# Kernel tuning notes

Hardware: AMD Instinct MI355X
Metric: run time of the kernel (lower is better)

The kernel has to match this reference:

```python
import jax, jax.numpy as jnp
import numpy as np

NUM_HEADS = 4


def setup_inputs() -> dict:
    key = jax.random.key(0)
    ks = jax.random.split(key, 12)
    N, E_edges, ND, ED, D, G = 50000, 800000, 128, 64, 256, 128
    h = jax.random.normal(ks[0], (N, ND), dtype=jnp.float32)
    edge_index = jax.random.randint(ks[1], (2, E_edges), 0, N)
    edge_attr = jax.random.normal(ks[2], (E_edges, ED), dtype=jnp.float32)
    batch = jnp.sort(jax.random.randint(ks[3], (N,), 0, G))
    node_w = jax.random.normal(ks[4], (D, ND), dtype=jnp.float32) / np.sqrt(ND)
    node_b = jnp.zeros((D,), dtype=jnp.float32)
    edge_w = jax.random.normal(ks[5], (D, ED), dtype=jnp.float32) / np.sqrt(ED)
    edge_b = jnp.zeros((D,), dtype=jnp.float32)
    query = jax.random.normal(ks[6], (1, D), dtype=jnp.float32)
    in_w = jax.random.normal(ks[7], (3 * D, D), dtype=jnp.float32) / np.sqrt(D)
    in_b = jnp.zeros((3 * D,), dtype=jnp.float32)
    out_w = jax.random.normal(ks[8], (D, D), dtype=jnp.float32) / np.sqrt(D)
    out_b = jnp.zeros((D,), dtype=jnp.float32)
    return {"h": h, "edge_index": edge_index, "edge_attr": edge_attr, "batch": batch,
            "num_graphs": G, "node_w": node_w, "node_b": node_b,
            "edge_w": edge_w, "edge_b": edge_b, "query": query,
            "in_w": in_w, "in_b": in_b, "out_w": out_w, "out_b": out_b}


def reference(h, edge_index, edge_attr, batch, num_graphs,
              node_w, node_b, edge_w, edge_b, query, in_w, in_b, out_w, out_b):
    N = h.shape[0]
    D = query.shape[-1]
    dh = D // NUM_HEADS
    G = num_graphs
    # node projection
    h_proj = h @ node_w.T + node_b  # [N, D]
    # scatter-mean edge features to source nodes
    row = edge_index[0]
    e_proj = edge_attr @ edge_w.T + edge_b  # [E, D]
    e_sum = jax.ops.segment_sum(e_proj, row, num_segments=N)
    cnt = jax.ops.segment_sum(jnp.ones((row.shape[0],), jnp.float32), row, num_segments=N)
    h_proj = h_proj + e_sum / jnp.maximum(cnt, 1.0)[:, None]
    # per-graph single-query multi-head attention (torch MultiheadAttention math)
    wq, wk, wv = in_w[:D], in_w[D:2 * D], in_w[2 * D:]
    bq, bk, bv = in_b[:D], in_b[D:2 * D], in_b[2 * D:]
    q = (query @ wq.T + bq).reshape(NUM_HEADS, dh)            # [H, dh]
    k = (h_proj @ wk.T + bk).reshape(N, NUM_HEADS, dh)        # [N, H, dh]
    v = (h_proj @ wv.T + bv).reshape(N, NUM_HEADS, dh)        # [N, H, dh]
    scores = jnp.einsum('hd,nhd->nh', q, k) / jnp.sqrt(jnp.float32(dh))  # [N, H]
    smax = jax.ops.segment_max(scores, batch, num_segments=G)  # [G, H]
    w = jnp.exp(scores - smax[batch])                          # [N, H]
    denom = jax.ops.segment_sum(w, batch, num_segments=G)      # [G, H]
    p = w / jnp.maximum(denom[batch], 1e-30)                   # [N, H]
    pooled = jax.ops.segment_sum(p[:, :, None] * v, batch, num_segments=G)  # [G, H, dh]
    out = pooled.reshape(G, 1, D) @ out_w.T + out_b            # [G, 1, D]
    return out
```

## Files before the change

kernel.cpp:

```cpp
#include <hip/hip_runtime.h>
#include <hip/hip_bf16.h>
#include <math.h>

#define NDIM 128
#define EDIM 64
#define DDIM 256
#define BM 32
#define APK_STRIDE 204
#define HPB_STRIDE 264
#define NSPLIT 4
#define CAP 96
#define NSWZ (8 * 12 * 64 * 8)

typedef __attribute__((ext_vector_type(8))) short short8;
typedef __attribute__((ext_vector_type(16))) float floatx16;

__device__ inline ushort f2bf(float x) {
    uint32_t u = __float_as_uint(x);
    uint32_t r = (u + 0x7fff + ((u >> 16) & 1)) >> 16;
    return (ushort)r;
}
__device__ inline float bf2f(ushort h) { return __uint_as_float(((uint32_t)h) << 16); }
__device__ inline uint32_t pack_hilo(float x) {
    ushort hi = f2bf(x);
    ushort lo = f2bf(x - bf2f(hi));
    return (uint32_t)hi | ((uint32_t)lo << 16);
}

__global__ __launch_bounds__(256) void k_setup(
    int* __restrict__ zero_p, int n_zero, int ZBLK,
    const float* __restrict__ node_w, const float* __restrict__ edge_w,
    ushort* __restrict__ whi, ushort* __restrict__ wlo,
    const float* __restrict__ query, const float* __restrict__ in_w,
    const float* __restrict__ in_b, float* __restrict__ qk, float* __restrict__ sb)
{
    const int tid = threadIdx.x;
    int b = blockIdx.x;
    if (b < ZBLK) {
        int i = b * 256 + tid;
        if (i < n_zero) zero_p[i] = 0;
        return;
    }
    b -= ZBLK;
    if (b < 192) {
        int idx = b * 256 + tid;
        int i = idx & 7;
        int l = (idx >> 3) & 63;
        int rest = idx >> 9;
        int s = rest % 12;
        int t2 = rest / 12;
        int k = s * 16 + (l >> 5) * 8 + i;
        int col = t2 * 32 + (l & 31);
        float val = (k < NDIM) ? node_w[(size_t)col * NDIM + k]
                               : edge_w[(size_t)col * EDIM + (k - NDIM)];
        ushort hi = f2bf(val);
        ushort lo = f2bf(val - bf2f(hi));
        whi[idx] = hi;
        wlo[idx] = lo;
        return;
    }
    __shared__ float q_s[DDIM];
    __shared__ float qv[DDIM];
    q_s[tid] = query[tid];
    __syncthreads();
    float acc = in_b[tid];
    const float* wq = in_w + (size_t)tid * DDIM;
    for (int i = 0; i < DDIM; ++i) acc += q_s[i] * wq[i];
    qv[tid] = acc;
    __syncthreads();
    for (int h = 0; h < 4; ++h) {
        float a = 0.f;
        for (int d = 0; d < 64; ++d)
            a += qv[h * 64 + d] * in_w[(size_t)(DDIM + h * 64 + d) * DDIM + tid];
        qk[h * DDIM + tid] = a;
    }
    if (tid < 4) {
        float a = 0.f;
        for (int d = 0; d < 64; ++d) a += qv[tid * 64 + d] * in_b[DDIM + tid * 64 + d];
        sb[tid] = a;
    }
}

__global__ __launch_bounds__(256) void k_scatter(
    const int* __restrict__ erow, int* __restrict__ fill,
    int* __restrict__ perm, int E)
{
    int e = blockIdx.x * 256 + threadIdx.x;
    if (e < E) {
        int r = erow[e];
        int pos = atomicAdd(&fill[r], 1);
        if (pos < CAP) perm[(size_t)r * CAP + pos] = e;
    }
}

__global__ __launch_bounds__(256) void k_agg(
    const float* __restrict__ edge_attr, const int* __restrict__ perm,
    const int* __restrict__ fill, float* __restrict__ agg, int N)
{
    int tid = threadIdx.x;
    int n = blockIdx.x * 4 + (tid >> 6);
    if (n >= N) return;
    int lane = tid & 63, seg = lane & 15, jg = lane >> 4;
    int s = n * CAP;
    int c = min(fill[n], CAP);
    float4 acc = make_float4(0.f, 0.f, 0.f, 0.f);
    int j = jg;
    for (; j + 12 < c; j += 16) {
        int e0 = perm[s + j];
        int e1 = perm[s + j + 4];
        int e2 = perm[s + j + 8];
        int e3 = perm[s + j + 12];
        float4 a0 = *reinterpret_cast<const float4*>(edge_attr + (size_t)e0 * EDIM + seg * 4);
        float4 a1 = *reinterpret_cast<const float4*>(edge_attr + (size_t)e1 * EDIM + seg * 4);
        float4 a2 = *reinterpret_cast<const float4*>(edge_attr + (size_t)e2 * EDIM + seg * 4);
        float4 a3 = *reinterpret_cast<const float4*>(edge_attr + (size_t)e3 * EDIM + seg * 4);
        acc.x += (a0.x + a1.x) + (a2.x + a3.x);
        acc.y += (a0.y + a1.y) + (a2.y + a3.y);
        acc.z += (a0.z + a1.z) + (a2.z + a3.z);
        acc.w += (a0.w + a1.w) + (a2.w + a3.w);
    }
    for (; j < c; j += 4) {
        int e0 = perm[s + j];
        float4 a0 = *reinterpret_cast<const float4*>(edge_attr + (size_t)e0 * EDIM + seg * 4);
        acc.x += a0.x; acc.y += a0.y; acc.z += a0.z; acc.w += a0.w;
    }
#pragma unroll
    for (int off = 16; off < 64; off <<= 1) {
        acc.x += __shfl_xor(acc.x, off);
        acc.y += __shfl_xor(acc.y, off);
        acc.z += __shfl_xor(acc.z, off);
        acc.w += __shfl_xor(acc.w, off);
    }
    if (jg == 0)
        *reinterpret_cast<float4*>(agg + (size_t)n * EDIM + seg * 4) = acc;
}

__global__ __launch_bounds__(256) void k_proj_mfma(
    const float* __restrict__ h, const float* __restrict__ agg, const int* __restrict__ fill,
    const ushort* __restrict__ whi, const ushort* __restrict__ wlo,
    const float* __restrict__ node_b, const float* __restrict__ edge_b,
    const float* __restrict__ qk, const float* __restrict__ sb,
    ushort* __restrict__ h_proj_bf, float* __restrict__ scores, int N)
{
    extern __shared__ char smem[];
    uint32_t* A_pk = (uint32_t*)smem;
    ushort*   hpbuf = (ushort*)smem;
    __shared__ float qk_s[4 * DDIM];
    __shared__ float cnt_s[BM];
    __shared__ float sb_s[4];

    const int tid = threadIdx.x;
    const int n0 = blockIdx.x * BM;

    if (tid < BM) {
        int n = n0 + tid;
        cnt_s[tid] = (n < N) ? (float)fill[n] : 0.f;
    }
    if (tid < 4) sb_s[tid] = sb[tid];
    for (int i = tid; i < 4 * DDIM; i += 256) qk_s[i] = qk[i];
    __syncthreads();

    const float4* h4 = reinterpret_cast<const float4*>(h);
#pragma unroll
    for (int it = 0; it < 4; ++it) {
        int idx4 = tid + 256 * it;
        int node = idx4 >> 5;
        int kq = idx4 & 31;
        float4 v = make_float4(0.f, 0.f, 0.f, 0.f);
        if (n0 + node < N) v = h4[(size_t)(n0 + node) * 32 + kq];
        uint32_t* dst = &A_pk[node * APK_STRIDE + kq * 4];
        dst[0] = pack_hilo(v.x); dst[1] = pack_hilo(v.y);
        dst[2] = pack_hilo(v.z); dst[3] = pack_hilo(v.w);
    }
    const float4* a4 = reinterpret_cast<const float4*>(agg);
#pragma unroll
    for (int it = 0; it < 2; ++it) {
        int idx4 = tid + 256 * it;
        int node = idx4 >> 4;
        int kq = idx4 & 15;
        float4 v = make_float4(0.f, 0.f, 0.f, 0.f);
        if (n0 + node < N) v = a4[(size_t)(n0 + node) * 16 + kq];
        float inv = 1.f / fmaxf(cnt_s[node], 1.f);
        uint32_t* dst = &A_pk[node * APK_STRIDE + NDIM + kq * 4];
        dst[0] = pack_hilo(v.x * inv); dst[1] = pack_hilo(v.y * inv);
        dst[2] = pack_hilo(v.z * inv); dst[3] = pack_hilo(v.w * inv);
    }
    __syncthreads();

    const int lane = tid & 63;
    const int w = tid >> 6;
    const int kg8 = (lane >> 5) * 8;
    const uint32_t* arow_p = &A_pk[(lane & 31) * APK_STRIDE];

    floatx16 acc[2];
#pragma unroll
    for (int t = 0; t < 2; ++t) acc[t] = 0.f;

#pragma unroll 4
    for (int s = 0; s < 12; ++s) {
        uint32_t au[8];
        *reinterpret_cast<uint4*>(&au[0]) = *reinterpret_cast<const uint4*>(&arow_p[s * 16 + kg8]);
        *reinterpret_cast<uint4*>(&au[4]) = *reinterpret_cast<const uint4*>(&arow_p[s * 16 + kg8 + 4]);
        short8 ahi, alo;
#pragma unroll
        for (int j = 0; j < 8; ++j) {
            ahi[j] = (short)(au[j] & 0xffffu);
            alo[j] = (short)(au[j] >> 16);
        }
#pragma unroll
        for (int t = 0; t < 2; ++t) {
            size_t boff = ((size_t)(((w * 2 + t) * 12 + s) * 64) + lane) * 8;
            short8 bhi = *reinterpret_cast<const short8*>(whi + boff);
            short8 blo = *reinterpret_cast<const short8*>(wlo + boff);
            acc[t] = __builtin_amdgcn_mfma_f32_32x32x16_bf16(ahi, bhi, acc[t], 0, 0, 0);
            acc[t] = __builtin_amdgcn_mfma_f32_32x32x16_bf16(ahi, blo, acc[t], 0, 0, 0);
            acc[t] = __builtin_amdgcn_mfma_f32_32x32x16_bf16(alo, bhi, acc[t], 0, 0, 0);
        }
    }
    __syncthreads();

#pragma unroll
    for (int t = 0; t < 2; ++t) {
        int colt = (w * 2 + t) * 32 + (lane & 31);
        float nb = node_b[colt];
        float eb = edge_b[colt];
#pragma unroll
        for (int r = 0; r < 16; ++r) {
            int row = (r & 3) + 8 * (r >> 2) + 4 * (lane >> 5);
            float fl = (cnt_s[row] >= 0.5f) ? 1.f : 0.f;
            float hp = acc[t][r] + nb + fl * eb;
            hpbuf[row * HPB_STRIDE + colt] = f2bf(hp);
        }
    }
    __syncthreads();

    {
        int row = tid >> 3, seg = tid & 7;
        int n = n0 + row;
        float s0 = 0.f, s1 = 0.f, s2 = 0.f, s3 = 0.f;
#pragma unroll
        for (int q = 0; q < 4; ++q) {
            short8 v = *reinterpret_cast<const short8*>(
                &hpbuf[row * HPB_STRIDE + seg * 32 + q * 8]);
#pragma unroll
            for (int jj = 0; jj < 8; ++jj) {
                float hv = bf2f((ushort)v[jj]);
                int dim = seg * 32 + q * 8 + jj;
                s0 += hv * qk_s[0 * DDIM + dim];
                s1 += hv * qk_s[1 * DDIM + dim];
                s2 += hv * qk_s[2 * DDIM + dim];
                s3 += hv * qk_s[3 * DDIM + dim];
            }
            if (n < N)
                *reinterpret_cast<short8*>(
                    &h_proj_bf[(size_t)n * DDIM + seg * 32 + q * 8]) = v;
        }
#pragma unroll
        for (int off = 1; off < 8; off <<= 1) {
            s0 += __shfl_xor(s0, off);
            s1 += __shfl_xor(s1, off);
            s2 += __shfl_xor(s2, off);
            s3 += __shfl_xor(s3, off);
        }
        if (seg == 0 && n < N) {
            scores[(size_t)n * 4 + 0] = (s0 + sb_s[0]) * 0.125f;
            scores[(size_t)n * 4 + 1] = (s1 + sb_s[1]) * 0.125f;
            scores[(size_t)n * 4 + 2] = (s2 + sb_s[2]) * 0.125f;
            scores[(size_t)n * 4 + 3] = (s3 + sb_s[3]) * 0.125f;
        }
    }
}

__global__ __launch_bounds__(256) void k_pool2(
    const ushort* __restrict__ h_proj_bf, const float* __restrict__ scores,
    const int* __restrict__ batch,
    float* __restrict__ pm, float* __restrict__ pd, float* __restrict__ phb, int N)
{
    __shared__ float sc_s[256 * 4];
    __shared__ float red_s[16];
    __shared__ float red[4][4][DDIM];

    const int b = blockIdx.x;
    const int g = b >> 2;
    const int part = b & 3;
    const int tid = threadIdx.x;
    const int lane = tid & 63;
    const int wave = tid >> 6;
    const int ng = tid >> 6;
    const int d0 = (tid & 63) * 4;

    int lo = 0, hi = N;
    while (lo < hi) { int mid = (lo + hi) >> 1; if (batch[mid] < g) lo = mid + 1; else hi = mid; }
    const int s = lo;
    hi = N;
    while (lo < hi) { int mid = (lo + hi) >> 1; if (batch[mid] < g + 1) lo = mid + 1; else hi = mid; }
    const int e = lo;
    const int len = e - s;
    const int cs = s + (len * part) / NSPLIT;
    const int ce = s + (len * (part + 1)) / NSPLIT;

    float m[4], dn[4];
    float hbv[4][4];
#pragma unroll
    for (int hh = 0; hh < 4; ++hh) {
        m[hh] = -INFINITY; dn[hh] = 0.f;
#pragma unroll
        for (int d = 0; d < 4; ++d) hbv[hh][d] = 0.f;
    }

    const int h = tid & 3;

    for (int c = cs; c < ce; c += 256) {
        int cn = min(256, ce - c);
        __syncthreads();
        if (tid < cn)
            *reinterpret_cast<float4*>(&sc_s[tid * 4]) =
                *reinterpret_cast<const float4*>(scores + (size_t)(c + tid) * 4);
        __syncthreads();

        float lm = -INFINITY;
        for (int n = tid >> 2; n < cn; n += 64) lm = fmaxf(lm, sc_s[n * 4 + h]);
#pragma unroll
        for (int off = 4; off < 64; off <<= 1) lm = fmaxf(lm, __shfl_xor(lm, off));
        if (lane < 4) red_s[wave * 4 + lane] = lm;
        __syncthreads();

        float nm[4];
#pragma unroll
        for (int hh = 0; hh < 4; ++hh) {
            float cm = fmaxf(fmaxf(red_s[hh], red_s[4 + hh]),
                             fmaxf(red_s[8 + hh], red_s[12 + hh]));
            nm[hh] = fmaxf(m[hh], cm);
            float sc = expf(m[hh] - nm[hh]);
            dn[hh] *= sc;
#pragma unroll
            for (int d = 0; d < 4; ++d) hbv[hh][d] *= sc;
            m[hh] = nm[hh];
        }
        __syncthreads();

        float mh = (h == 0) ? nm[0] : (h == 1) ? nm[1] : (h == 2) ? nm[2] : nm[3];
        float ld = 0.f;
        for (int idx = tid; idx < cn * 4; idx += 256) {
            float wv = expf(sc_s[idx] - mh);
            sc_s[idx] = wv;
            ld += wv;
        }
#pragma unroll
        for (int off = 4; off < 64; off <<= 1) ld += __shfl_xor(ld, off);
        __syncthreads();
        if (lane < 4) red_s[wave * 4 + lane] = ld;
        __syncthreads();
#pragma unroll
        for (int hh = 0; hh < 4; ++hh)
            dn[hh] += red_s[hh] + red_s[4 + hh] + red_s[8 + hh] + red_s[12 + hh];

#pragma unroll 2
        for (int nb = 0; nb < cn; nb += 4) {
            int ln = nb + ng;
            bool valid = ln < cn;
            float4 w4 = make_float4(0.f, 0.f, 0.f, 0.f);
            ushort4 hv = make_ushort4(0, 0, 0, 0);
            if (valid) {
                w4 = *reinterpret_cast<const float4*>(&sc_s[ln * 4]);
                hv = *reinterpret_cast<const ushort4*>(
                    &h_proj_bf[(size_t)(c + ln) * DDIM + d0]);
            }
            float vx = bf2f(hv.x), vy = bf2f(hv.y), vz = bf2f(hv.z), vw = bf2f(hv.w);
            hbv[0][0] += w4.x * vx; hbv[1][0] += w4.y * vx; hbv[2][0] += w4.z * vx; hbv[3][0] += w4.w * vx;
            hbv[0][1] += w4.x * vy; hbv[1][1] += w4.y * vy; hbv[2][1] += w4.z * vy; hbv[3][1] += w4.w * vy;
            hbv[0][2] += w4.x * vz; hbv[1][2] += w4.y * vz; hbv[2][2] += w4.z * vz; hbv[3][2] += w4.w * vz;
            hbv[0][3] += w4.x * vw; hbv[1][3] += w4.y * vw; hbv[2][3] += w4.z * vw; hbv[3][3] += w4.w * vw;
        }
    }

    __syncthreads();
#pragma unroll
    for (int hh = 0; hh < 4; ++hh)
#pragma unroll
        for (int d = 0; d < 4; ++d)
            red[ng][hh][d0 + d] = hbv[hh][d];
    __syncthreads();

    if (tid < 4) { pm[b * 4 + tid] = m[tid]; pd[b * 4 + tid] = dn[tid]; }
#pragma unroll
    for (int hh = 0; hh < 4; ++hh)
        phb[(size_t)(b * 4 + hh) * DDIM + tid] =
            red[0][hh][tid] + red[1][hh][tid] + red[2][hh][tid] + red[3][hh][tid];
}

__global__ __launch_bounds__(256) void k_out(
    const float* __restrict__ pm, const float* __restrict__ pd, const float* __restrict__ phb,
    const float* __restrict__ in_w, const float* __restrict__ in_b,
    const float* __restrict__ out_w, const float* __restrict__ out_b,
    float* __restrict__ out)
{
    __shared__ float hb_s[4 * DDIM];
    __shared__ float po_s[DDIM];

    const int g = blockIdx.x;
    const int tid = threadIdx.x;
    const int b0 = NSPLIT * g;

    float M[4], dnm[4], sc[NSPLIT][4];
#pragma unroll
    for (int hh = 0; hh < 4; ++hh) {
        float Mh = -INFINITY;
#pragma unroll
        for (int p = 0; p < NSPLIT; ++p) Mh = fmaxf(Mh, pm[(b0 + p) * 4 + hh]);
        M[hh] = Mh;
        float d = 0.f;
#pragma unroll
        for (int p = 0; p < NSPLIT; ++p) {
            float mp = pm[(b0 + p) * 4 + hh];
            float scp = (mp == -INFINITY) ? 0.f : expf(mp - Mh);
            sc[p][hh] = scp;
            d += pd[(b0 + p) * 4 + hh] * scp;
        }
        dnm[hh] = d;
    }
    const float has = (M[0] > -INFINITY) ? 1.f : 0.f;

#pragma unroll
    for (int hh = 0; hh < 4; ++hh) {
        float hb = 0.f;
#pragma unroll
        for (int p = 0; p < NSPLIT; ++p)
            hb += phb[(size_t)((b0 + p) * 4 + hh) * DDIM + tid] * sc[p][hh];
        hb_s[hh * DDIM + tid] = hb / fmaxf(dnm[hh], 1e-30f);
    }
    __syncthreads();

    const int jh = tid >> 6;
    const float* wv_row = in_w + (size_t)(2 * DDIM + tid) * DDIM;
    const float* hbr = &hb_s[jh * DDIM];
    float p = 0.f;
    for (int i = 0; i < DDIM; i += 4) {
        float4 a = *reinterpret_cast<const float4*>(hbr + i);
        float4 bb = *reinterpret_cast<const float4*>(wv_row + i);
        p += a.x * bb.x + a.y * bb.y + a.z * bb.z + a.w * bb.w;
    }
    p = (p + in_b[2 * DDIM + tid]) * has;
    po_s[tid] = p;
    __syncthreads();

    const float* ow_row = out_w + (size_t)tid * DDIM;
    float o = out_b[tid];
    for (int i = 0; i < DDIM; i += 4) {
        float4 a = *reinterpret_cast<const float4*>(&po_s[i]);
        float4 bb = *reinterpret_cast<const float4*>(ow_row + i);
        o += a.x * bb.x + a.y * bb.y + a.z * bb.z + a.w * bb.w;
    }
    out[(size_t)g * DDIM + tid] = o;
}

extern "C" void kernel_launch(void* const* d_in, const int* in_sizes, int n_in,
                              void* d_out, int out_size, void* d_ws, size_t ws_size,
                              hipStream_t stream) {
    const float* h         = (const float*)d_in[0];
    const int*   edge_idx  = (const int*)d_in[1];
    const float* edge_attr = (const float*)d_in[2];
    const int*   batch     = (const int*)d_in[3];
    const float* node_w    = (const float*)d_in[5];
    const float* node_b    = (const float*)d_in[6];
    const float* edge_w    = (const float*)d_in[7];
    const float* edge_b    = (const float*)d_in[8];
    const float* query     = (const float*)d_in[9];
    const float* in_w      = (const float*)d_in[10];
    const float* in_b      = (const float*)d_in[11];
    const float* out_w     = (const float*)d_in[12];
    const float* out_b     = (const float*)d_in[13];
    float* out = (float*)d_out;

    const int N = in_sizes[0] / NDIM;
    const int E = in_sizes[2] / EDIM;
    const int G = out_size / DDIM;

    char* ws = (char*)d_ws;
    size_t off = 0;
    auto alloc = [&](size_t bytes) { void* p = ws + off; off += (bytes + 255) & ~(size_t)255; return p; };

    int*    fill       = (int*)alloc((size_t)N * 4);
    int*    perm       = (int*)alloc((size_t)N * CAP * 4);
    float*  agg        = (float*)alloc((size_t)N * EDIM * 4);
    ushort* h_proj_bf  = (ushort*)alloc((size_t)N * DDIM * 2);
    float*  scores     = (float*)alloc((size_t)N * 4 * 4);
    ushort* whi        = (ushort*)alloc((size_t)NSWZ * 2);
    ushort* wlo        = (ushort*)alloc((size_t)NSWZ * 2);
    float*  qk         = (float*)alloc(4 * DDIM * 4);
    float*  sb         = (float*)alloc(16 * 4);
    float*  pm         = (float*)alloc((size_t)NSPLIT * G * 4 * 4);
    float*  pd         = (float*)alloc((size_t)NSPLIT * G * 4 * 4);
    float*  phb        = (float*)alloc((size_t)NSPLIT * G * 4 * DDIM * 4);

    const int ZBLK = (N + 255) / 256;
    k_setup<<<ZBLK + 192 + 1, 256, 0, stream>>>(
        fill, N, ZBLK, node_w, edge_w, whi, wlo, query, in_w, in_b, qk, sb);

    k_scatter<<<(E + 255) / 256, 256, 0, stream>>>(edge_idx, fill, perm, E);
    k_agg<<<(N + 3) / 4, 256, 0, stream>>>(edge_attr, perm, fill, agg, N);

    const int ldsA = BM * APK_STRIDE * 4;
    k_proj_mfma<<<(N + BM - 1) / BM, 256, ldsA, stream>>>(
        h, agg, fill, whi, wlo, node_b, edge_b, qk, sb, h_proj_bf, scores, N);

    k_pool2<<<NSPLIT * G, 256, 0, stream>>>(h_proj_bf, scores, batch, pm, pd, phb, N);
    k_out<<<G, 256, 0, stream>>>(pm, pd, phb, in_w, in_b, out_w, out_b, out);
}
```

Measured before the change: 206.2 us.

## Fuse edge-feature gather aggregation into the MFMA projection kernel

Removes the separate k_agg kernel and the agg intermediate buffer. The projection kernel now gathers each node's incoming edge rows through perm directly, with 8 threads per node each summing 8 columns, and writes the mean straight into shared memory. This saves one launch plus the write and reread of an N×64 float buffer. In exchange, the gather loses the 4-way edge-parallel split per node, so per-thread loops are longer, latency hiding in a kernel with heavy shared-memory use may be weaker, and load imbalance comes from varying degree.

```diff
diff --git a/kernel.cpp b/kernel.cpp
--- a/kernel.cpp
+++ b/kernel.cpp
@@ -93,50 +93,9 @@
     }
 }
 
-__global__ __launch_bounds__(256) void k_agg(
-    const float* __restrict__ edge_attr, const int* __restrict__ perm,
-    const int* __restrict__ fill, float* __restrict__ agg, int N)
-{
-    int tid = threadIdx.x;
-    int n = blockIdx.x * 4 + (tid >> 6);
-    if (n >= N) return;
-    int lane = tid & 63, seg = lane & 15, jg = lane >> 4;
-    int s = n * CAP;
-    int c = min(fill[n], CAP);
-    float4 acc = make_float4(0.f, 0.f, 0.f, 0.f);
-    int j = jg;
-    for (; j + 12 < c; j += 16) {
-        int e0 = perm[s + j];
-        int e1 = perm[s + j + 4];
-        int e2 = perm[s + j + 8];
-        int e3 = perm[s + j + 12];
-        float4 a0 = *reinterpret_cast<const float4*>(edge_attr + (size_t)e0 * EDIM + seg * 4);
-        float4 a1 = *reinterpret_cast<const float4*>(edge_attr + (size_t)e1 * EDIM + seg * 4);
-        float4 a2 = *reinterpret_cast<const float4*>(edge_attr + (size_t)e2 * EDIM + seg * 4);
-        float4 a3 = *reinterpret_cast<const float4*>(edge_attr + (size_t)e3 * EDIM + seg * 4);
-        acc.x += (a0.x + a1.x) + (a2.x + a3.x);
-        acc.y += (a0.y + a1.y) + (a2.y + a3.y);
-        acc.z += (a0.z + a1.z) + (a2.z + a3.z);
-        acc.w += (a0.w + a1.w) + (a2.w + a3.w);
-    }
-    for (; j < c; j += 4) {
-        int e0 = perm[s + j];
-        float4 a0 = *reinterpret_cast<const float4*>(edge_attr + (size_t)e0 * EDIM + seg * 4);
-        acc.x += a0.x; acc.y += a0.y; acc.z += a0.z; acc.w += a0.w;
-    }
-#pragma unroll
-    for (int off = 16; off < 64; off <<= 1) {
-        acc.x += __shfl_xor(acc.x, off);
-        acc.y += __shfl_xor(acc.y, off);
-        acc.z += __shfl_xor(acc.z, off);
-        acc.w += __shfl_xor(acc.w, off);
-    }
-    if (jg == 0)
-        *reinterpret_cast<float4*>(agg + (size_t)n * EDIM + seg * 4) = acc;
-}
-
-__global__ __launch_bounds__(256) void k_proj_mfma(
-    const float* __restrict__ h, const float* __restrict__ agg, const int* __restrict__ fill,
+__global__ __launch_bounds__(256) void k_projagg(
+    const float* __restrict__ h, const float* __restrict__ edge_attr,
+    const int* __restrict__ perm, const int* __restrict__ fill,
     const ushort* __restrict__ whi, const ushort* __restrict__ wlo,
     const float* __restrict__ node_b, const float* __restrict__ edge_b,
     const float* __restrict__ qk, const float* __restrict__ sb,
@@ -158,7 +117,6 @@
     }
     if (tid < 4) sb_s[tid] = sb[tid];
     for (int i = tid; i < 4 * DDIM; i += 256) qk_s[i] = qk[i];
-    __syncthreads();
 
     const float4* h4 = reinterpret_cast<const float4*>(h);
 #pragma unroll
@@ -172,18 +130,54 @@
         dst[0] = pack_hilo(v.x); dst[1] = pack_hilo(v.y);
         dst[2] = pack_hilo(v.z); dst[3] = pack_hilo(v.w);
     }
-    const float4* a4 = reinterpret_cast<const float4*>(agg);
-#pragma unroll
-    for (int it = 0; it < 2; ++it) {
-        int idx4 = tid + 256 * it;
-        int node = idx4 >> 4;
-        int kq = idx4 & 15;
-        float4 v = make_float4(0.f, 0.f, 0.f, 0.f);
-        if (n0 + node < N) v = a4[(size_t)(n0 + node) * 16 + kq];
+
+    __syncthreads();
+
+    {
+        int node = tid >> 3;
+        int seg8 = tid & 7;
+        int n = n0 + node;
+        float a0 = 0.f, a1 = 0.f, a2 = 0.f, a3 = 0.f;
+        float a4 = 0.f, a5 = 0.f, a6 = 0.f, a7 = 0.f;
+        if (n < N) {
+            int s = n * CAP;
+            int c = min((int)cnt_s[node], CAP);
+            const float* ea = edge_attr + seg8 * 8;
+            int j = 0;
+            for (; j + 3 < c; j += 4) {
+                int e0 = perm[s + j], e1 = perm[s + j + 1];
+                int e2 = perm[s + j + 2], e3 = perm[s + j + 3];
+                float4 v0a = *reinterpret_cast<const float4*>(ea + (size_t)e0 * EDIM);
+                float4 v0b = *reinterpret_cast<const float4*>(ea + (size_t)e0 * EDIM + 4);
+                float4 v1a = *reinterpret_cast<const float4*>(ea + (size_t)e1 * EDIM);
+                float4 v1b = *reinterpret_cast<const float4*>(ea + (size_t)e1 * EDIM + 4);
+                float4 v2a = *reinterpret_cast<const float4*>(ea + (size_t)e2 * EDIM);
+                float4 v2b = *reinterpret_cast<const float4*>(ea + (size_t)e2 * EDIM + 4);
+                float4 v3a = *reinterpret_cast<const float4*>(ea + (size_t)e3 * EDIM);
+                float4 v3b = *reinterpret_cast<const float4*>(ea + (size_t)e3 * EDIM + 4);
+                a0 += (v0a.x + v1a.x) + (v2a.x + v3a.x);
+                a1 += (v0a.y + v1a.y) + (v2a.y + v3a.y);
+                a2 += (v0a.z + v1a.z) + (v2a.z + v3a.z);
+                a3 += (v0a.w + v1a.w) + (v2a.w + v3a.w);
+                a4 += (v0b.x + v1b.x) + (v2b.x + v3b.x);
+                a5 += (v0b.y + v1b.y) + (v2b.y + v3b.y);
+                a6 += (v0b.z + v1b.z) + (v2b.z + v3b.z);
+                a7 += (v0b.w + v1b.w) + (v2b.w + v3b.w);
+            }
+            for (; j < c; ++j) {
+                int e0 = perm[s + j];
+                float4 va = *reinterpret_cast<const float4*>(ea + (size_t)e0 * EDIM);
+                float4 vb = *reinterpret_cast<const float4*>(ea + (size_t)e0 * EDIM + 4);
+                a0 += va.x; a1 += va.y; a2 += va.z; a3 += va.w;
+                a4 += vb.x; a5 += vb.y; a6 += vb.z; a7 += vb.w;
+            }
+        }
         float inv = 1.f / fmaxf(cnt_s[node], 1.f);
-        uint32_t* dst = &A_pk[node * APK_STRIDE + NDIM + kq * 4];
-        dst[0] = pack_hilo(v.x * inv); dst[1] = pack_hilo(v.y * inv);
-        dst[2] = pack_hilo(v.z * inv); dst[3] = pack_hilo(v.w * inv);
+        uint32_t* dst = &A_pk[node * APK_STRIDE + NDIM + seg8 * 8];
+        dst[0] = pack_hilo(a0 * inv); dst[1] = pack_hilo(a1 * inv);
+        dst[2] = pack_hilo(a2 * inv); dst[3] = pack_hilo(a3 * inv);
+        dst[4] = pack_hilo(a4 * inv); dst[5] = pack_hilo(a5 * inv);
+        dst[6] = pack_hilo(a6 * inv); dst[7] = pack_hilo(a7 * inv);
     }
     __syncthreads();
 
@@ -482,7 +476,6 @@
 
     int*    fill       = (int*)alloc((size_t)N * 4);
     int*    perm       = (int*)alloc((size_t)N * CAP * 4);
-    float*  agg        = (float*)alloc((size_t)N * EDIM * 4);
     ushort* h_proj_bf  = (ushort*)alloc((size_t)N * DDIM * 2);
     float*  scores     = (float*)alloc((size_t)N * 4 * 4);
     ushort* whi        = (ushort*)alloc((size_t)NSWZ * 2);
@@ -498,11 +491,11 @@
         fill, N, ZBLK, node_w, edge_w, whi, wlo, query, in_w, in_b, qk, sb);
 
     k_scatter<<<(E + 255) / 256, 256, 0, stream>>>(edge_idx, fill, perm, E);
-    k_agg<<<(N + 3) / 4, 256, 0, stream>>>(edge_attr, perm, fill, agg, N);
 
     const int ldsA = BM * APK_STRIDE * 4;
-    k_proj_mfma<<<(N + BM - 1) / BM, 256, ldsA, stream>>>(
-        h, agg, fill, whi, wlo, node_b, edge_b, qk, sb, h_proj_bf, scores, N);
+    k_projagg<<<(N + BM - 1) / BM, 256, ldsA, stream>>>(
+        h, edge_attr, perm, fill, whi, wlo, node_b, edge_b, qk, sb,
+        h_proj_bf, scores, N);
 
     k_pool2<<<NSPLIT * G, 256, 0, stream>>>(h_proj_bf, scores, batch, pm, pd, phb, N);
     k_out<<<G, 256, 0, stream>>>(pm, pd, phb, in_w, in_b, out_w, out_b, out);
```

After: 209.3 us. Within noise of the previous version (+1.5%).
